# Kernel optimization log

Hardware: AMD Instinct MI355X
Metric: run time of the kernel (lower is better)

Reference implementation:

```python
import math
import jax, jax.numpy as jnp
from jax import lax
import numpy as np

SCORE_THR = 0.5
IOU_THR = 0.7
MIN_SIZE = 1.0
BBOX_CLIP = math.log(1000.0 / 16.0)

FEAT_SIZES = [100, 50, 25, 13, 7]
STRIDES = [8, 16, 32, 64, 128]
RATIOS = (0.5, 1.0, 2.0)
C = 256
A = 3
N = 2


def _make_priors(fs, stride):
    base = stride * 4.0
    ys, xs = np.meshgrid(np.arange(fs), np.arange(fs), indexing='ij')
    cx = (xs + 0.5) * stride
    cy = (ys + 0.5) * stride
    pri = []
    for r in RATIOS:
        w = base / np.sqrt(r)
        h = base * np.sqrt(r)
        pri.append(np.stack([cx - w / 2, cy - h / 2, cx + w / 2, cy + h / 2], axis=-1))
    pri = np.stack(pri, axis=2)  # (fs, fs, A, 4): H,W,A order matches permute/reshape
    return jnp.asarray(pri.reshape(-1, 4), dtype=jnp.float32)


def setup_inputs():
    key = jax.random.key(0)
    ks = jax.random.split(key, 8)
    inp = {}
    for i, fs in enumerate(FEAT_SIZES):
        inp[f'fmap{i}'] = jax.random.normal(jax.random.fold_in(ks[0], i), (N, C, fs, fs), dtype=jnp.float32)
        inp[f'priors{i}'] = _make_priors(fs, STRIDES[i])
    sc = 0.02
    inp['conv_w'] = jax.random.normal(ks[1], (C, C, 3, 3), jnp.float32) * sc
    inp['conv_b'] = jnp.zeros((C,), jnp.float32)
    inp['log_w'] = jax.random.normal(ks[2], (A, C, 1, 1), jnp.float32) * sc
    inp['log_b'] = jnp.zeros((A,), jnp.float32)
    inp['reg_w'] = jax.random.normal(ks[3], (A * 4, C, 1, 1), jnp.float32) * sc
    inp['reg_b'] = jnp.zeros((A * 4,), jnp.float32)
    inp['imsizes'] = jnp.full((N, 2), 800, dtype=jnp.int32)  # (h, w) per image
    inp['lvtop'] = 500
    inp['imtop'] = 100
    return inp


def _conv(x, w, b, pad):
    y = lax.conv_general_dilated(x, w, (1, 1), pad, dimension_numbers=('NCHW', 'OIHW', 'NCHW'))
    return y + b[None, :, None, None]


def _decode(reg, pri):
    pw = pri[..., 2] - pri[..., 0]
    ph = pri[..., 3] - pri[..., 1]
    pcx = pri[..., 0] + 0.5 * pw
    pcy = pri[..., 1] + 0.5 * ph
    dx, dy = reg[..., 0], reg[..., 1]
    dw = jnp.minimum(reg[..., 2], BBOX_CLIP)
    dh = jnp.minimum(reg[..., 3], BBOX_CLIP)
    cx = dx * pw + pcx
    cy = dy * ph + pcy
    w = jnp.exp(dw) * pw
    h = jnp.exp(dh) * ph
    return jnp.stack([cx - 0.5 * w, cy - 0.5 * h, cx + 0.5 * w, cy + 0.5 * h], axis=-1)


def _head(x, priors, conv_w, conv_b, log_w, log_b, reg_w, reg_b, lvtop):
    n = x.shape[0]
    h = jax.nn.relu(_conv(x, conv_w, conv_b, 'SAME'))
    reg = _conv(h, reg_w, reg_b, 'VALID').transpose(0, 2, 3, 1).reshape(n, -1, 4)
    log = _conv(h, log_w, log_b, 'VALID').transpose(0, 2, 3, 1).reshape(n, -1)
    k = min(lvtop, log.shape[1])
    vals, top = lax.top_k(log, k)                           # (n, k)
    reg = jnp.take_along_axis(reg, top[..., None], axis=1)  # (n, k, 4)
    pri = priors[top]                                       # (n, k, 4)
    return _decode(reg, pri), vals, k


def _box_iou(a, b):
    area_a = (a[:, 2] - a[:, 0]) * (a[:, 3] - a[:, 1])
    area_b = (b[:, 2] - b[:, 0]) * (b[:, 3] - b[:, 1])
    lt = jnp.maximum(a[:, None, :2], b[None, :, :2])
    rb = jnp.minimum(a[:, None, 2:], b[None, :, 2:])
    wh = jnp.clip(rb - lt, 0.0)
    inter = wh[..., 0] * wh[..., 1]
    return inter / (area_a[:, None] + area_b[None, :] - inter + 1e-9)


def _forward(fmaps, priors, conv_w, conv_b, log_w, log_b, reg_w, reg_b, imsizes, lvtop, imtop):
    tups = [_head(x, p, conv_w, conv_b, log_w, log_b, reg_w, reg_b, lvtop)
            for x, p in zip(fmaps, priors)]
    boxes = jnp.concatenate([t[0] for t in tups], axis=1)                 # (n, D, 4)
    obj = jax.nn.sigmoid(jnp.concatenate([t[1] for t in tups], axis=1))   # (n, D)
    lvlen = jnp.asarray([t[2] for t in tups])
    n, D = obj.shape
    boxes = boxes.reshape(-1, 4)
    obj = obj.reshape(-1)
    K = n * D
    imidx = jnp.arange(K) // D
    valid = obj >= SCORE_THR                                # score filter (masked, not nonzero)
    hw = imsizes[imidx].astype(jnp.float32)                 # (K, 2) = (h, w)
    x1 = jnp.clip(boxes[:, 0], 0.0, hw[:, 1])
    y1 = jnp.clip(boxes[:, 1], 0.0, hw[:, 0])
    x2 = jnp.clip(boxes[:, 2], 0.0, hw[:, 1])
    y2 = jnp.clip(boxes[:, 3], 0.0, hw[:, 0])
    boxes = jnp.stack([x1, y1, x2, y2], axis=-1)
    valid &= (x2 - x1 >= MIN_SIZE) & (y2 - y1 >= MIN_SIZE)  # remove_small
    lvidx = jnp.searchsorted(jnp.cumsum(lvlen), jnp.arange(K) % D, side='right')
    groups = imidx * 10 + lvidx
    scores = jnp.where(valid, obj, -jnp.inf)
    order = jnp.argsort(-scores)                            # global score order; groups gate suppression
    b, g, v, ii = boxes[order], groups[order], valid[order], imidx[order]
    iou = _box_iou(b, b)                                    # (K, K)
    ar = jnp.arange(K)
    def body(i, keep):
        sup = (iou[i] > IOU_THR) & (g == g[i]) & (ar > i)
        return jnp.where(keep[i], keep & ~sup, keep)
    keep = lax.fori_loop(0, K, body, v)                     # greedy batched NMS
    def select(i):
        m = keep & (ii == i)
        sel = jnp.argsort(~m)[:imtop]                       # stable: kept boxes in score order
        val = m[sel]
        bx = jnp.where(val[:, None], b[sel], 0.0)
        ix = jnp.where(val, i, -1)
        return bx, ix
    bx, ix = jax.vmap(select)(jnp.arange(n))
    return bx.reshape(n * imtop, 4), ix.reshape(n * imtop)


def reference(fmap0, fmap1, fmap2, fmap3, fmap4, priors0, priors1, priors2, priors3, priors4,
              conv_w, conv_b, log_w, log_b, reg_w, reg_b, imsizes, lvtop, imtop):
    return _forward([fmap0, fmap1, fmap2, fmap3, fmap4],
                    [priors0, priors1, priors2, priors3, priors4],
                    conv_w, conv_b, log_w, log_b, reg_w, reg_b, imsizes, lvtop, imtop)
```

## Files before the change

kernel.cpp:

```cpp
#include <hip/hip_runtime.h>
#include <math.h>


#define N_IMG 2
#define C_CH  256
#define D_PER 2147
#define K_TOT 4294
#define K_PAD 8192
#define CONV_BLOCKS 1912
#define CPX 239

__constant__ int c_Ml[5]     = {30000, 7500, 1875, 507, 147};
__constant__ int c_kl[5]     = {500, 500, 500, 500, 147};
__constant__ int c_lvoff[5]  = {0, 500, 1000, 1500, 2000};
__constant__ int c_logoff[5] = {0, 60000, 75000, 78750, 79764};
__constant__ int c_regoff[5] = {0, 240000, 300000, 315000, 319056};
__constant__ int c_fs[5]     = {100, 50, 25, 13, 7};
__constant__ int c_npt[5]    = {13, 7, 4, 2, 1};
__constant__ int c_E[5]      = {10000, 2500, 625, 169, 49};
__constant__ int c_cumbl[6]  = {0, 1352, 1744, 1872, 1904, 1912};
__constant__ int c_hcum[6]   = {0, 157, 197, 207, 210, 211};
__constant__ size_t c_hoff[5] = {0, 5120000, 6400000, 6720000, 6806528};

__global__ void transpose_w_kernel(const float* __restrict__ w,
                                   double* __restrict__ wT2) {
  int i = blockIdx.x * 256 + threadIdx.x;
  if (i >= 589824) return;
  int q = i % 2304;
  int slab = i / 2304;
  int cobi = slab >> 6, ch = slab & 63;
  int ci = q / 576;
  int rem = q % 576;
  int tap = rem / 64, co = rem & 63;
  wT2[i] =
      (double)w[(size_t)(cobi * 64 + co) * 2304 + (ch * 4 + ci) * 9 + tap];
}

template <typename T>
__global__ __launch_bounds__(256) void conv_fused_kernel(
    const float* __restrict__ x0, const float* __restrict__ x1,
    const float* __restrict__ x2, const float* __restrict__ x3,
    const float* __restrict__ x4, const double* __restrict__ wT2,
    const float* __restrict__ bias, T* __restrict__ h) {
  __shared__ double s_in[4 * 120];
  __shared__ double s_w[2304];
  int tid = threadIdx.x;
  int bid = (blockIdx.x & 7) * CPX + (blockIdx.x >> 3);
  int l = 0;
  while (bid >= c_cumbl[l + 1]) ++l;
  int r = bid - c_cumbl[l];
  int fs = c_fs[l], npt = c_npt[l];
  int tiles = npt * npt;
  int tile = r % tiles;
  int cn = r / tiles;
  int cobi = cn & 3, n = cn >> 2;
  int ptx = tile % npt, pty = tile / npt;
  int px0 = ptx * 8, py0 = pty * 8;
  int E = fs * fs;
  const float* xl;
  switch (l) {
    case 0: xl = x0; break;
    case 1: xl = x1; break;
    case 2: xl = x2; break;
    case 3: xl = x3; break;
    default: xl = x4; break;
  }
  const float* xn = xl + (size_t)n * C_CH * E;
  T* hl = h + c_hoff[l];

  int tpx = tid & 15, tco = tid >> 4;
  int prow = tpx >> 1, pcol0 = (tpx & 1) * 4;

  int in_dst[2], in_src[2];
#pragma unroll
  for (int it = 0; it < 2; ++it) {
    int idx = tid + it * 256;
    in_dst[it] = -1;
    in_src[it] = -1;
    if (idx < 400) {
      int ci = idx / 100, rr2 = idx % 100;
      int hy = rr2 / 10, hx = rr2 % 10;
      int gy = py0 - 1 + hy, gx = px0 - 1 + hx;
      in_dst[it] = ci * 120 + hy * 12 + hx;
      if (gy >= 0 && gy < fs && gx >= 0 && gx < fs)
        in_src[it] = ci * E + gy * fs + gx;
    }
  }

  double acc[4][4];
#pragma unroll
  for (int i = 0; i < 4; i++)
#pragma unroll
    for (int j = 0; j < 4; j++) acc[i][j] = 0.0;

  const double2* wsrc0 = (const double2*)(wT2 + (size_t)cobi * 64 * 2304);

  for (int ch = 0; ch < 64; ++ch) {
    const float* xc = xn + (size_t)ch * 4 * E;
#pragma unroll
    for (int it = 0; it < 2; ++it) {
      if (in_dst[it] >= 0) {
        float v = (in_src[it] >= 0) ? xc[in_src[it]] : 0.f;
        s_in[in_dst[it]] = (double)v;
      }
    }
    {
      const double2* src = wsrc0 + (size_t)ch * 1152;
      double2* dst = (double2*)s_w;
#pragma unroll
      for (int k = 0; k < 5; k++) {
        int idx = tid + k * 256;
        if (idx < 1152) dst[idx] = src[idx];
      }
    }
    __syncthreads();
#pragma unroll
    for (int ci = 0; ci < 4; ++ci) {
      const double* inp = &s_in[ci * 120];
      const double* wpb = &s_w[ci * 576];
#pragma unroll
      for (int ky = 0; ky < 3; ++ky) {
        const double* ip = inp + (prow + ky) * 12 + pcol0;
        double2 a0 = *(const double2*)ip;
        double2 a1 = *(const double2*)(ip + 2);
        double2 a2 = *(const double2*)(ip + 4);
        double d6[6];
        d6[0] = a0.x; d6[1] = a0.y; d6[2] = a1.x;
        d6[3] = a1.y; d6[4] = a2.x; d6[5] = a2.y;
#pragma unroll
        for (int kx = 0; kx < 3; ++kx) {
          const double* wp = wpb + (ky * 3 + kx) * 64 + tco * 4;
          double2 wA = *(const double2*)wp;
          double2 wB = *(const double2*)(wp + 2);
          double w0 = wA.x, w1 = wA.y, w2 = wB.x, w3 = wB.y;
#pragma unroll
          for (int pj = 0; pj < 4; pj++) {
            double iv = d6[pj + kx];
            acc[0][pj] = fma(w0, iv, acc[0][pj]);
            acc[1][pj] = fma(w1, iv, acc[1][pj]);
            acc[2][pj] = fma(w2, iv, acc[2][pj]);
            acc[3][pj] = fma(w3, iv, acc[3][pj]);
          }
        }
      }
    }
    __syncthreads();
  }

  int gy = py0 + prow;
  if (gy < fs) {
#pragma unroll
    for (int coi = 0; coi < 4; ++coi) {
      int co = cobi * 64 + tco * 4 + coi;
      double bb = (double)bias[co];
#pragma unroll
      for (int pj = 0; pj < 4; pj++) {
        int gx = px0 + pcol0 + pj;
        if (gx < fs) {
          double v = acc[coi][pj] + bb;
          hl[((size_t)n * C_CH + co) * E + gy * fs + gx] = (T)fmax(v, 0.0);
        }
      }
    }
  }
}

template <typename T>
__global__ __launch_bounds__(256) void heads_fused_kernel(
    const T* __restrict__ h, const float* __restrict__ logw,
    const float* __restrict__ logb, const float* __restrict__ regw,
    const float* __restrict__ regb, double* __restrict__ logits,
    double* __restrict__ regs) {
  __shared__ float s_wh[256][16];
  __shared__ double s_red[4][15][64];
  int tid = threadIdx.x;
  int n = blockIdx.y;
  int cidx = blockIdx.x;
  int l = 0;
  while (cidx >= c_hcum[l + 1]) ++l;
  int chunk = cidx - c_hcum[l];
  int E = c_E[l];
  int px0 = chunk * 64;
  const T* hl = h + c_hoff[l];
  double* logits_l = logits + c_logoff[l];
  double* regs_l = regs + c_regoff[l];

  for (int idx = tid; idx < 4096; idx += 256) {
    int c = idx >> 4, j = idx & 15;
    float v = 0.f;
    if (j < 3) v = logw[j * 256 + c];
    else if (j < 15) v = regw[(j - 3) * 256 + c];
    s_wh[c][j] = v;
  }
  __syncthreads();

  int p = tid & 63, c4 = tid >> 6;
  int pix = px0 + p;
  bool act = pix < E;
  double acc[15];
#pragma unroll
  for (int j = 0; j < 15; j++) acc[j] = 0.0;
  if (act) {
    const T* hp = hl + ((size_t)n * C_CH + c4 * 64) * E + pix;
    for (int cc = 0; cc < 64; ++cc) {
      double hv = (double)hp[(size_t)cc * E];
      const float* wr = &s_wh[c4 * 64 + cc][0];
#pragma unroll
      for (int j = 0; j < 15; j++)
        acc[j] = fma((double)wr[j], hv, acc[j]);
    }
  }
#pragma unroll
  for (int j = 0; j < 15; j++) s_red[c4][j][p] = acc[j];
  __syncthreads();
  if (act) {
    int M = E * 3;
    for (int j = c4; j < 15; j += 4) {
      double v = s_red[0][j][p] + s_red[1][j][p] + s_red[2][j][p] +
                 s_red[3][j][p];
      if (j < 3) {
        logits_l[(size_t)n * M + pix * 3 + j] = v + (double)logb[j];
      } else {
        int rj = j - 3, a = rj >> 2, coord = rj & 3;
        regs_l[((size_t)n * M + pix * 3 + a) * 4 + coord] =
            v + (double)regb[rj];
      }
    }
  }
}

__device__ __forceinline__ unsigned long long d2key(double v) {
  unsigned long long ub = (unsigned long long)__double_as_longlong(v);
  return (ub >> 63) ? ~ub : (ub | 0x8000000000000000ull);
}

#define TK_CH 30
__global__ __launch_bounds__(1024) void topk_kernel(
    const double* __restrict__ logits, int* __restrict__ cand_anchor) {
  int bid = blockIdx.x;
  int n = bid / 5, l = bid % 5;
  int M = c_Ml[l], k = c_kl[l];
  const double* lg = logits + c_logoff[l] + (size_t)n * M;
  int tid = threadIdx.x;
  __shared__ int histw[16][256];
  __shared__ int hist[256];
  __shared__ unsigned long long s_prefix;
  __shared__ int s_r;
  if (tid == 0) { s_prefix = 0ull; s_r = k; }

  int chunk = (M + 1023) >> 10;
  int i0 = tid * chunk, i1 = min(M, i0 + chunk);
  int cnt = i1 - i0;
  if (cnt < 0) cnt = 0;
  unsigned long long kv[TK_CH];
#pragma unroll
  for (int q = 0; q < TK_CH; q++)
    if (q < cnt) kv[q] = d2key(lg[i0 + q]);
  int wid = tid >> 6;
  __syncthreads();

  for (int pass = 0; pass < 8; ++pass) {
    int shift = 56 - pass * 8;
    for (int i = tid; i < 4096; i += 1024) ((int*)histw)[i] = 0;
    __syncthreads();
    unsigned long long pfx = s_prefix;
    int rr = s_r;
#pragma unroll
    for (int q = 0; q < TK_CH; q++) {
      if (q < cnt) {
        unsigned long long u = kv[q];
        if (pass == 0 || (u >> (shift + 8)) == pfx)
          atomicAdd(&histw[wid][(int)((u >> shift) & 255ull)], 1);
      }
    }
    __syncthreads();
    if (tid < 256) {
      int s = 0;
#pragma unroll
      for (int w = 0; w < 16; w++) s += histw[w][tid];
      hist[tid] = s;
    }
    __syncthreads();
    if (tid == 0) {
      int s = 0, beta = 0;
      for (int b = 255; b >= 0; --b) {
        if (s + hist[b] >= rr) { beta = b; break; }
        s += hist[b];
      }
      s_prefix = (pfx << 8) | (unsigned long long)beta;
      s_r = rr - s;
    }
    __syncthreads();
  }
  unsigned long long T = s_prefix;
  int need = s_r;
  int cgt = 0, ceq = 0;
#pragma unroll
  for (int q = 0; q < TK_CH; q++) {
    if (q < cnt) {
      cgt += (kv[q] > T);
      ceq += (kv[q] == T);
    }
  }
  __shared__ int sgt[1024], seq[1024];
  sgt[tid] = cgt;
  seq[tid] = ceq;
  __syncthreads();
  for (int o = 1; o < 1024; o <<= 1) {
    int a = (tid >= o) ? sgt[tid - o] : 0;
    int b2 = (tid >= o) ? seq[tid - o] : 0;
    __syncthreads();
    sgt[tid] += a;
    seq[tid] += b2;
    __syncthreads();
  }
  int gt_total = sgt[1023];
  int pg = sgt[tid] - cgt, pe = seq[tid] - ceq;
  int base = n * D_PER + c_lvoff[l];
#pragma unroll
  for (int q = 0; q < TK_CH; q++) {
    if (q < cnt) {
      unsigned long long u = kv[q];
      if (u > T) {
        cand_anchor[base + (pg++)] = i0 + q;
      } else if (u == T) {
        if (pe < need) cand_anchor[base + gt_total + pe] = i0 + q;
        pe++;
      }
    }
  }
}

__global__ __launch_bounds__(256) void decode_kernel(
    const int* __restrict__ cand_anchor, const double* __restrict__ logits,
    const double* __restrict__ regs, const float* __restrict__ p0,
    const float* __restrict__ p1, const float* __restrict__ p2,
    const float* __restrict__ p3, const float* __restrict__ p4,
    const int* __restrict__ imsizes, double* __restrict__ cand_score,
    double* __restrict__ cand_box, int* __restrict__ cand_group,
    int* __restrict__ cand_valid) {
  int s = blockIdx.x * 256 + threadIdx.x;
  if (s >= K_TOT) return;
  int n = s / D_PER;
  int rr = s % D_PER;
  int l = (rr < 2000) ? (rr / 500) : 4;
  int aidx = cand_anchor[s];
  int M = c_Ml[l];
  const float* pp;
  switch (l) {
    case 0: pp = p0; break;
    case 1: pp = p1; break;
    case 2: pp = p2; break;
    case 3: pp = p3; break;
    default: pp = p4; break;
  }
  double lv = logits[c_logoff[l] + (size_t)n * M + aidx];
  double obj = 1.0 / (1.0 + exp(-lv));
  const double* rp = regs + c_regoff[l] + ((size_t)n * M + aidx) * 4;
  const float* pr = pp + (size_t)aidx * 4;
  double px1 = pr[0], py1 = pr[1], px2 = pr[2], py2 = pr[3];
  double pw = px2 - px1, ph = py2 - py1;
  double pcx = px1 + 0.5 * pw, pcy = py1 + 0.5 * ph;
  const double BCLIP = 4.1351665567423560;
  double dx = rp[0], dy = rp[1];
  double dw = fmin(rp[2], BCLIP), dh = fmin(rp[3], BCLIP);
  double cx = dx * pw + pcx, cy = dy * ph + pcy;
  double w = exp(dw) * pw, hh = exp(dh) * ph;
  double x1 = cx - 0.5 * w, y1 = cy - 0.5 * hh;
  double x2 = cx + 0.5 * w, y2 = cy + 0.5 * hh;
  double imh = (double)imsizes[n * 2 + 0], imw = (double)imsizes[n * 2 + 1];
  x1 = fmin(fmax(x1, 0.0), imw);
  x2 = fmin(fmax(x2, 0.0), imw);
  y1 = fmin(fmax(y1, 0.0), imh);
  y2 = fmin(fmax(y2, 0.0), imh);
  bool valid = (obj >= 0.5) && ((x2 - x1) >= 1.0) && ((y2 - y1) >= 1.0);
  cand_box[(size_t)s * 4 + 0] = x1;
  cand_box[(size_t)s * 4 + 1] = y1;
  cand_box[(size_t)s * 4 + 2] = x2;
  cand_box[(size_t)s * 4 + 3] = y2;
  cand_score[s] = valid ? obj : -(double)INFINITY;
  cand_group[s] = n * 5 + l;
  cand_valid[s] = valid ? 1 : 0;
}

__global__ __launch_bounds__(1024) void sort_kernel(
    const double* __restrict__ cand_score, int* __restrict__ order) {
  __shared__ unsigned long long key[K_PAD];
  int tid = threadIdx.x;
  for (int i = tid; i < K_PAD; i += 1024) {
    unsigned long long kk = 0ull;
    if (i < K_TOT) {
      unsigned long long u = d2key(cand_score[i]);
      kk = (u & ~0x1FFFull) | (unsigned long long)i;
    }
    key[i] = kk;
  }
  __syncthreads();
  for (int k = 2; k <= K_PAD; k <<= 1) {
    for (int j = k >> 1; j > 0; j >>= 1) {
      for (int i = tid; i < K_PAD; i += 1024) {
        int ixj = i ^ j;
        if (ixj > i) {
          unsigned long long a = key[i], b = key[ixj];
          bool sw = ((i & k) == 0) ? (a < b) : (a > b);
          if (sw) { key[i] = b; key[ixj] = a; }
        }
      }
      __syncthreads();
    }
  }
  for (int i = tid; i < K_TOT; i += 1024)
    order[i] = (int)(key[i] & 0x1FFFull);
}

__global__ __launch_bounds__(256) void gather_kernel(
    const int* __restrict__ order, const double* __restrict__ cand_box,
    const int* __restrict__ cand_group, const int* __restrict__ cand_valid,
    double* __restrict__ box_s, int* __restrict__ grp_s,
    int* __restrict__ img_s, int* __restrict__ valid_s,
    int* __restrict__ keep_s) {
  int i = blockIdx.x * 256 + threadIdx.x;
  if (i >= K_TOT) return;
  int s = order[i];
#pragma unroll
  for (int q = 0; q < 4; q++)
    box_s[(size_t)i * 4 + q] = cand_box[(size_t)s * 4 + q];
  int g = cand_group[s];
  grp_s[i] = g;
  img_s[i] = g / 5;
  valid_s[i] = cand_valid[s];
  keep_s[i] = 0;
}

#define MAXM 512
__global__ __launch_bounds__(256) void nms_kernel(
    const double* __restrict__ box_s, const int* __restrict__ grp_s,
    const int* __restrict__ valid_s, int* __restrict__ keep_s) {
  int g = blockIdx.x;
  int tid = threadIdx.x;
  __shared__ int cnt[256];
  __shared__ int mem[MAXM];
  __shared__ double bx[MAXM][4];
  __shared__ unsigned long long mask[MAXM][8];
  const int chunk = (K_TOT + 255) / 256;
  int i0 = tid * chunk, i1 = min(K_TOT, i0 + chunk);
  int c = 0;
  for (int i = i0; i < i1; ++i) c += (grp_s[i] == g && valid_s[i]);
  cnt[tid] = c;
  __syncthreads();
  for (int o = 1; o < 256; o <<= 1) {
    int v = (tid >= o) ? cnt[tid - o] : 0;
    __syncthreads();
    cnt[tid] += v;
    __syncthreads();
  }
  int off = cnt[tid] - c;
  int m = cnt[255];
  for (int i = i0; i < i1; ++i)
    if (grp_s[i] == g && valid_s[i]) mem[off++] = i;
  __syncthreads();
  for (int t = tid; t < m; t += 256) {
    int i = mem[t];
#pragma unroll
    for (int q = 0; q < 4; q++) bx[t][q] = box_s[(size_t)i * 4 + q];
  }
  __syncthreads();
  for (int i = tid; i < m; i += 256) {
    unsigned long long row[8] = {0, 0, 0, 0, 0, 0, 0, 0};
    double ax1 = bx[i][0], ay1 = bx[i][1], ax2 = bx[i][2], ay2 = bx[i][3];
    double areaA = (ax2 - ax1) * (ay2 - ay1);
    for (int j = i + 1; j < m; ++j) {
      double bx1 = bx[j][0], by1 = bx[j][1], bx2 = bx[j][2], by2 = bx[j][3];
      double areaB = (bx2 - bx1) * (by2 - by1);
      double lx = fmax(ax1, bx1), ly = fmax(ay1, by1);
      double rx = fmin(ax2, bx2), ry = fmin(ay2, by2);
      double iw = fmax(rx - lx, 0.0), ih = fmax(ry - ly, 0.0);
      double inter = iw * ih;
      double iou = inter / (areaA + areaB - inter + 1e-9);
      if (iou > 0.7) row[j >> 6] |= (1ull << (j & 63));
    }
#pragma unroll
    for (int w2 = 0; w2 < 8; ++w2) mask[i][w2] = row[w2];
  }
  __syncthreads();
  if (tid == 0) {
    unsigned long long remv[8] = {0, 0, 0, 0, 0, 0, 0, 0};
    for (int i = 0; i < m; ++i) {
      if (!((remv[i >> 6] >> (i & 63)) & 1ull)) {
        keep_s[mem[i]] = 1;
#pragma unroll
        for (int w2 = 0; w2 < 8; ++w2) remv[w2] |= mask[i][w2];
      }
    }
  }
}

__global__ __launch_bounds__(256) void select_kernel(
    const double* __restrict__ box_s, const int* __restrict__ img_s,
    const int* __restrict__ keep_s, float* __restrict__ out) {
  int n = blockIdx.x;
  int tid = threadIdx.x;
  __shared__ int cnt[256];
  const int chunk = (K_TOT + 255) / 256;
  int i0 = tid * chunk, i1 = min(K_TOT, i0 + chunk);
  int c = 0;
  for (int i = i0; i < i1; ++i) c += (keep_s[i] && img_s[i] == n);
  cnt[tid] = c;
  __syncthreads();
  for (int o = 1; o < 256; o <<= 1) {
    int v = (tid >= o) ? cnt[tid - o] : 0;
    __syncthreads();
    cnt[tid] += v;
    __syncthreads();
  }
  int pos = cnt[tid] - c;
  int total = cnt[255];
  for (int i = i0; i < i1; ++i) {
    if (keep_s[i] && img_s[i] == n) {
      if (pos < 100) {
#pragma unroll
        for (int q = 0; q < 4; q++)
          out[(n * 100 + pos) * 4 + q] = (float)box_s[(size_t)i * 4 + q];
        out[800 + n * 100 + pos] = (float)n;
      }
      pos++;
    }
  }
  for (int p = total + tid; p < 100; p += 256) {
#pragma unroll
    for (int q = 0; q < 4; q++) out[(n * 100 + p) * 4 + q] = 0.0f;
    out[800 + n * 100 + p] = -1.0f;
  }
}

extern "C" void kernel_launch(void* const* d_in, const int* in_sizes, int n_in,
                              void* d_out, int out_size, void* d_ws,
                              size_t ws_size, hipStream_t stream) {
  (void)in_sizes; (void)n_in; (void)out_size;
  const float* fmap[5];
  const float* priors[5];
  for (int l = 0; l < 5; l++) {
    fmap[l] = (const float*)d_in[2 * l];
    priors[l] = (const float*)d_in[2 * l + 1];
  }
  const float* conv_w = (const float*)d_in[10];
  const float* conv_b = (const float*)d_in[11];
  const float* log_w = (const float*)d_in[12];
  const float* log_b = (const float*)d_in[13];
  const float* reg_w = (const float*)d_in[14];
  const float* reg_b = (const float*)d_in[15];
  const int* imsizes = (const int*)d_in[16];
  float* out = (float*)d_out;

  bool f64h = ws_size >= (size_t)66000000;

  char* base = (char*)d_ws;
  size_t off = 0;
  auto alloc = [&](size_t bytes) -> void* {
    off = (off + 255) & ~(size_t)255;
    void* p = base + off;
    off += bytes;
    return p;
  };
  double* wT2 = (double*)alloc(589824ull * 8);
  void* hraw = alloc(6831616ull * (f64h ? 8 : 4));
  double* logits = (double*)alloc(80058ull * 8);
  double* regs = (double*)alloc(320232ull * 8);
  int* cand_anchor = (int*)alloc(K_TOT * 4);
  double* cand_score = (double*)alloc(K_TOT * 8);
  double* cand_box = (double*)alloc((size_t)K_TOT * 4 * 8);
  int* cand_group = (int*)alloc(K_TOT * 4);
  int* cand_valid = (int*)alloc(K_TOT * 4);
  int* order = (int*)alloc(K_TOT * 4);
  double* box_s = (double*)alloc((size_t)K_TOT * 4 * 8);
  int* grp_s = (int*)alloc(K_TOT * 4);
  int* img_s = (int*)alloc(K_TOT * 4);
  int* valid_s = (int*)alloc(K_TOT * 4);
  int* keep_s = (int*)alloc(K_TOT * 4);

  transpose_w_kernel<<<2304, 256, 0, stream>>>(conv_w, wT2);

  if (f64h) {
    conv_fused_kernel<double><<<CONV_BLOCKS, 256, 0, stream>>>(
        fmap[0], fmap[1], fmap[2], fmap[3], fmap[4], wT2, conv_b,
        (double*)hraw);
    heads_fused_kernel<double><<<dim3(211, 2), 256, 0, stream>>>(
        (double*)hraw, log_w, log_b, reg_w, reg_b, logits, regs);
  } else {
    conv_fused_kernel<float><<<CONV_BLOCKS, 256, 0, stream>>>(
        fmap[0], fmap[1], fmap[2], fmap[3], fmap[4], wT2, conv_b,
        (float*)hraw);
    heads_fused_kernel<float><<<dim3(211, 2), 256, 0, stream>>>(
        (float*)hraw, log_w, log_b, reg_w, reg_b, logits, regs);
  }
  topk_kernel<<<10, 1024, 0, stream>>>(logits, cand_anchor);
  decode_kernel<<<(K_TOT + 255) / 256, 256, 0, stream>>>(
      cand_anchor, logits, regs, priors[0], priors[1], priors[2], priors[3],
      priors[4], imsizes, cand_score, cand_box, cand_group, cand_valid);
  sort_kernel<<<1, 1024, 0, stream>>>(cand_score, order);
  gather_kernel<<<(K_TOT + 255) / 256, 256, 0, stream>>>(
      order, cand_box, cand_group, cand_valid, box_s, grp_s, img_s, valid_s,
      keep_s);
  nms_kernel<<<10, 256, 0, stream>>>(box_s, grp_s, valid_s, keep_s);
  select_kernel<<<2, 256, 0, stream>>>(box_s, img_s, keep_s, out);
}
```

Measured before the change: 1.199 ms.

## Fuse topk, decode, per-group sort and NMS into one kernel; merge-select per image

Replaces the topk, decode, global 8192-wide bitonic sort, gather and NMS kernels with one kernel per (image, level) group. Each block does its own top-k, decodes boxes into shared memory, sorts 512 keys locally and runs NMS, then writes the kept boxes in order. A 5-way merge in select_kernel then builds the per-image top 100. The conv input tile stride also changes from 12 to 13 doubles, presumably to cut LDS bank conflicts, which gives up the aligned double2 loads. The intent is to cut launch count, global round-trips and the large single-block sort in the post-processing tail.

```diff
diff --git a/kernel.cpp b/kernel.cpp
--- a/kernel.cpp
+++ b/kernel.cpp
@@ -6,13 +6,11 @@
 #define C_CH  256
 #define D_PER 2147
 #define K_TOT 4294
-#define K_PAD 8192
 #define CONV_BLOCKS 1912
 #define CPX 239
 
 __constant__ int c_Ml[5]     = {30000, 7500, 1875, 507, 147};
 __constant__ int c_kl[5]     = {500, 500, 500, 500, 147};
-__constant__ int c_lvoff[5]  = {0, 500, 1000, 1500, 2000};
 __constant__ int c_logoff[5] = {0, 60000, 75000, 78750, 79764};
 __constant__ int c_regoff[5] = {0, 240000, 300000, 315000, 319056};
 __constant__ int c_fs[5]     = {100, 50, 25, 13, 7};
@@ -42,7 +40,7 @@
     const float* __restrict__ x2, const float* __restrict__ x3,
     const float* __restrict__ x4, const double* __restrict__ wT2,
     const float* __restrict__ bias, T* __restrict__ h) {
-  __shared__ double s_in[4 * 120];
+  __shared__ double s_in[4 * 130];
   __shared__ double s_w[2304];
   int tid = threadIdx.x;
   int bid = (blockIdx.x & 7) * CPX + (blockIdx.x >> 3);
@@ -81,7 +79,7 @@
       int ci = idx / 100, rr2 = idx % 100;
       int hy = rr2 / 10, hx = rr2 % 10;
       int gy = py0 - 1 + hy, gx = px0 - 1 + hx;
-      in_dst[it] = ci * 120 + hy * 12 + hx;
+      in_dst[it] = ci * 130 + hy * 13 + hx;
       if (gy >= 0 && gy < fs && gx >= 0 && gx < fs)
         in_src[it] = ci * E + gy * fs + gx;
     }
@@ -99,10 +97,8 @@
     const float* xc = xn + (size_t)ch * 4 * E;
 #pragma unroll
     for (int it = 0; it < 2; ++it) {
-      if (in_dst[it] >= 0) {
-        float v = (in_src[it] >= 0) ? xc[in_src[it]] : 0.f;
-        s_in[in_dst[it]] = (double)v;
-      }
+      if (in_dst[it] >= 0)
+        s_in[in_dst[it]] = (in_src[it] >= 0) ? (double)xc[in_src[it]] : 0.0;
     }
     {
       const double2* src = wsrc0 + (size_t)ch * 1152;
@@ -116,17 +112,14 @@
     __syncthreads();
 #pragma unroll
     for (int ci = 0; ci < 4; ++ci) {
-      const double* inp = &s_in[ci * 120];
+      const double* inp = &s_in[ci * 130];
       const double* wpb = &s_w[ci * 576];
 #pragma unroll
       for (int ky = 0; ky < 3; ++ky) {
-        const double* ip = inp + (prow + ky) * 12 + pcol0;
-        double2 a0 = *(const double2*)ip;
-        double2 a1 = *(const double2*)(ip + 2);
-        double2 a2 = *(const double2*)(ip + 4);
+        const double* ip = inp + (prow + ky) * 13 + pcol0;
         double d6[6];
-        d6[0] = a0.x; d6[1] = a0.y; d6[2] = a1.x;
-        d6[3] = a1.y; d6[4] = a2.x; d6[5] = a2.y;
+#pragma unroll
+        for (int j = 0; j < 6; j++) d6[j] = ip[j];
 #pragma unroll
         for (int kx = 0; kx < 3; ++kx) {
           const double* wp = wpb + (ky * 3 + kx) * 64 + tco * 4;
@@ -235,17 +228,40 @@
 }
 
 #define TK_CH 30
-__global__ __launch_bounds__(1024) void topk_kernel(
-    const double* __restrict__ logits, int* __restrict__ cand_anchor) {
+union TkShared {
+  struct {
+    int histw[16][256];
+    int hist[256];
+    int sgt[1024];
+    int seq[1024];
+  } a;
+  struct {
+    unsigned long long u[512];
+    int idx[512];
+    int keep[512];
+    int ps[512];
+    int m;
+    double bx[512][4];
+    unsigned long long mask[512][8];
+  } b;
+};
+
+__global__ __launch_bounds__(1024) void topk_nms_kernel(
+    const double* __restrict__ logits, const double* __restrict__ regs,
+    const float* __restrict__ p0, const float* __restrict__ p1,
+    const float* __restrict__ p2, const float* __restrict__ p3,
+    const float* __restrict__ p4, const int* __restrict__ imsizes,
+    double* __restrict__ g_box, unsigned long long* __restrict__ g_u,
+    int* __restrict__ g_cnt) {
+  __shared__ TkShared sh;
+  __shared__ int s_sel[512];
+  __shared__ unsigned long long s_prefix;
+  __shared__ int s_r;
   int bid = blockIdx.x;
   int n = bid / 5, l = bid % 5;
   int M = c_Ml[l], k = c_kl[l];
   const double* lg = logits + c_logoff[l] + (size_t)n * M;
   int tid = threadIdx.x;
-  __shared__ int histw[16][256];
-  __shared__ int hist[256];
-  __shared__ unsigned long long s_prefix;
-  __shared__ int s_r;
   if (tid == 0) { s_prefix = 0ull; s_r = k; }
 
   int chunk = (M + 1023) >> 10;
@@ -261,7 +277,7 @@
 
   for (int pass = 0; pass < 8; ++pass) {
     int shift = 56 - pass * 8;
-    for (int i = tid; i < 4096; i += 1024) ((int*)histw)[i] = 0;
+    for (int i = tid; i < 4096; i += 1024) ((int*)sh.a.histw)[i] = 0;
     __syncthreads();
     unsigned long long pfx = s_prefix;
     int rr = s_r;
@@ -270,22 +286,22 @@
       if (q < cnt) {
         unsigned long long u = kv[q];
         if (pass == 0 || (u >> (shift + 8)) == pfx)
-          atomicAdd(&histw[wid][(int)((u >> shift) & 255ull)], 1);
+          atomicAdd(&sh.a.histw[wid][(int)((u >> shift) & 255ull)], 1);
       }
     }
     __syncthreads();
     if (tid < 256) {
       int s = 0;
 #pragma unroll
-      for (int w = 0; w < 16; w++) s += histw[w][tid];
-      hist[tid] = s;
+      for (int w = 0; w < 16; w++) s += sh.a.histw[w][tid];
+      sh.a.hist[tid] = s;
     }
     __syncthreads();
     if (tid == 0) {
       int s = 0, beta = 0;
       for (int b = 255; b >= 0; --b) {
-        if (s + hist[b] >= rr) { beta = b; break; }
-        s += hist[b];
+        if (s + sh.a.hist[b] >= rr) { beta = b; break; }
+        s += sh.a.hist[b];
       }
       s_prefix = (pfx << 8) | (unsigned long long)beta;
       s_r = rr - s;
@@ -302,50 +318,33 @@
       ceq += (kv[q] == T);
     }
   }
-  __shared__ int sgt[1024], seq[1024];
-  sgt[tid] = cgt;
-  seq[tid] = ceq;
+  sh.a.sgt[tid] = cgt;
+  sh.a.seq[tid] = ceq;
   __syncthreads();
   for (int o = 1; o < 1024; o <<= 1) {
-    int a = (tid >= o) ? sgt[tid - o] : 0;
-    int b2 = (tid >= o) ? seq[tid - o] : 0;
-    __syncthreads();
-    sgt[tid] += a;
-    seq[tid] += b2;
-    __syncthreads();
-  }
-  int gt_total = sgt[1023];
-  int pg = sgt[tid] - cgt, pe = seq[tid] - ceq;
-  int base = n * D_PER + c_lvoff[l];
+    int a = (tid >= o) ? sh.a.sgt[tid - o] : 0;
+    int b2 = (tid >= o) ? sh.a.seq[tid - o] : 0;
+    __syncthreads();
+    sh.a.sgt[tid] += a;
+    sh.a.seq[tid] += b2;
+    __syncthreads();
+  }
+  int gt_total = sh.a.sgt[1023];
+  int pg = sh.a.sgt[tid] - cgt, pe = sh.a.seq[tid] - ceq;
 #pragma unroll
   for (int q = 0; q < TK_CH; q++) {
     if (q < cnt) {
       unsigned long long u = kv[q];
       if (u > T) {
-        cand_anchor[base + (pg++)] = i0 + q;
+        s_sel[pg++] = i0 + q;
       } else if (u == T) {
-        if (pe < need) cand_anchor[base + gt_total + pe] = i0 + q;
+        if (pe < need) s_sel[gt_total + pe] = i0 + q;
         pe++;
       }
     }
   }
-}
-
-__global__ __launch_bounds__(256) void decode_kernel(
-    const int* __restrict__ cand_anchor, const double* __restrict__ logits,
-    const double* __restrict__ regs, const float* __restrict__ p0,
-    const float* __restrict__ p1, const float* __restrict__ p2,
-    const float* __restrict__ p3, const float* __restrict__ p4,
-    const int* __restrict__ imsizes, double* __restrict__ cand_score,
-    double* __restrict__ cand_box, int* __restrict__ cand_group,
-    int* __restrict__ cand_valid) {
-  int s = blockIdx.x * 256 + threadIdx.x;
-  if (s >= K_TOT) return;
-  int n = s / D_PER;
-  int rr = s % D_PER;
-  int l = (rr < 2000) ? (rr / 500) : 4;
-  int aidx = cand_anchor[s];
-  int M = c_Ml[l];
+  __syncthreads();
+
   const float* pp;
   switch (l) {
     case 0: pp = p0; break;
@@ -354,123 +353,79 @@
     case 3: pp = p3; break;
     default: pp = p4; break;
   }
-  double lv = logits[c_logoff[l] + (size_t)n * M + aidx];
-  double obj = 1.0 / (1.0 + exp(-lv));
-  const double* rp = regs + c_regoff[l] + ((size_t)n * M + aidx) * 4;
-  const float* pr = pp + (size_t)aidx * 4;
-  double px1 = pr[0], py1 = pr[1], px2 = pr[2], py2 = pr[3];
-  double pw = px2 - px1, ph = py2 - py1;
-  double pcx = px1 + 0.5 * pw, pcy = py1 + 0.5 * ph;
+  const double* regs_l = regs + c_regoff[l];
+  double imh = (double)imsizes[n * 2 + 0], imw = (double)imsizes[n * 2 + 1];
   const double BCLIP = 4.1351665567423560;
-  double dx = rp[0], dy = rp[1];
-  double dw = fmin(rp[2], BCLIP), dh = fmin(rp[3], BCLIP);
-  double cx = dx * pw + pcx, cy = dy * ph + pcy;
-  double w = exp(dw) * pw, hh = exp(dh) * ph;
-  double x1 = cx - 0.5 * w, y1 = cy - 0.5 * hh;
-  double x2 = cx + 0.5 * w, y2 = cy + 0.5 * hh;
-  double imh = (double)imsizes[n * 2 + 0], imw = (double)imsizes[n * 2 + 1];
-  x1 = fmin(fmax(x1, 0.0), imw);
-  x2 = fmin(fmax(x2, 0.0), imw);
-  y1 = fmin(fmax(y1, 0.0), imh);
-  y2 = fmin(fmax(y2, 0.0), imh);
-  bool valid = (obj >= 0.5) && ((x2 - x1) >= 1.0) && ((y2 - y1) >= 1.0);
-  cand_box[(size_t)s * 4 + 0] = x1;
-  cand_box[(size_t)s * 4 + 1] = y1;
-  cand_box[(size_t)s * 4 + 2] = x2;
-  cand_box[(size_t)s * 4 + 3] = y2;
-  cand_score[s] = valid ? obj : -(double)INFINITY;
-  cand_group[s] = n * 5 + l;
-  cand_valid[s] = valid ? 1 : 0;
-}
-
-__global__ __launch_bounds__(1024) void sort_kernel(
-    const double* __restrict__ cand_score, int* __restrict__ order) {
-  __shared__ unsigned long long key[K_PAD];
-  int tid = threadIdx.x;
-  for (int i = tid; i < K_PAD; i += 1024) {
-    unsigned long long kk = 0ull;
-    if (i < K_TOT) {
-      unsigned long long u = d2key(cand_score[i]);
-      kk = (u & ~0x1FFFull) | (unsigned long long)i;
-    }
-    key[i] = kk;
-  }
-  __syncthreads();
-  for (int k = 2; k <= K_PAD; k <<= 1) {
-    for (int j = k >> 1; j > 0; j >>= 1) {
-      for (int i = tid; i < K_PAD; i += 1024) {
-        int ixj = i ^ j;
+  if (tid < 512) {
+    unsigned long long key = 0ull;
+    sh.b.idx[tid] = tid;
+    sh.b.keep[tid] = 0;
+    if (tid < k) {
+      int aidx = s_sel[tid];
+      double lv = lg[aidx];
+      double obj = 1.0 / (1.0 + exp(-lv));
+      const double* rp = regs_l + ((size_t)n * M + aidx) * 4;
+      const float* pr = pp + (size_t)aidx * 4;
+      double px1 = pr[0], py1 = pr[1], px2 = pr[2], py2 = pr[3];
+      double pw = px2 - px1, ph = py2 - py1;
+      double pcx = px1 + 0.5 * pw, pcy = py1 + 0.5 * ph;
+      double dx = rp[0], dy = rp[1];
+      double dw = fmin(rp[2], BCLIP), dh = fmin(rp[3], BCLIP);
+      double cx = dx * pw + pcx, cy = dy * ph + pcy;
+      double w = exp(dw) * pw, hh = exp(dh) * ph;
+      double x1 = cx - 0.5 * w, y1 = cy - 0.5 * hh;
+      double x2 = cx + 0.5 * w, y2 = cy + 0.5 * hh;
+      x1 = fmin(fmax(x1, 0.0), imw);
+      x2 = fmin(fmax(x2, 0.0), imw);
+      y1 = fmin(fmax(y1, 0.0), imh);
+      y2 = fmin(fmax(y2, 0.0), imh);
+      bool valid = (obj >= 0.5) && ((x2 - x1) >= 1.0) && ((y2 - y1) >= 1.0);
+      sh.b.bx[tid][0] = x1;
+      sh.b.bx[tid][1] = y1;
+      sh.b.bx[tid][2] = x2;
+      sh.b.bx[tid][3] = y2;
+      if (valid) key = d2key(obj);
+    }
+    sh.b.u[tid] = key;
+  }
+  if (tid == 0) sh.b.m = 0;
+  __syncthreads();
+
+  for (int kk = 2; kk <= 512; kk <<= 1) {
+    for (int j = kk >> 1; j > 0; j >>= 1) {
+      if (tid < 512) {
+        int i = tid, ixj = i ^ j;
         if (ixj > i) {
-          unsigned long long a = key[i], b = key[ixj];
-          bool sw = ((i & k) == 0) ? (a < b) : (a > b);
-          if (sw) { key[i] = b; key[ixj] = a; }
+          unsigned long long ua = sh.b.u[i], ub = sh.b.u[ixj];
+          int ia = sh.b.idx[i], ib = sh.b.idx[ixj];
+          bool up = ((i & kk) == 0);
+          bool aAfterB = (ua < ub) || (ua == ub && ia > ib);
+          bool sw = up ? aAfterB : !aAfterB && (ua != ub || ia != ib);
+          if (sw) {
+            sh.b.u[i] = ub; sh.b.u[ixj] = ua;
+            sh.b.idx[i] = ib; sh.b.idx[ixj] = ia;
+          }
         }
       }
       __syncthreads();
     }
   }
-  for (int i = tid; i < K_TOT; i += 1024)
-    order[i] = (int)(key[i] & 0x1FFFull);
-}
-
-__global__ __launch_bounds__(256) void gather_kernel(
-    const int* __restrict__ order, const double* __restrict__ cand_box,
-    const int* __restrict__ cand_group, const int* __restrict__ cand_valid,
-    double* __restrict__ box_s, int* __restrict__ grp_s,
-    int* __restrict__ img_s, int* __restrict__ valid_s,
-    int* __restrict__ keep_s) {
-  int i = blockIdx.x * 256 + threadIdx.x;
-  if (i >= K_TOT) return;
-  int s = order[i];
-#pragma unroll
-  for (int q = 0; q < 4; q++)
-    box_s[(size_t)i * 4 + q] = cand_box[(size_t)s * 4 + q];
-  int g = cand_group[s];
-  grp_s[i] = g;
-  img_s[i] = g / 5;
-  valid_s[i] = cand_valid[s];
-  keep_s[i] = 0;
-}
-
-#define MAXM 512
-__global__ __launch_bounds__(256) void nms_kernel(
-    const double* __restrict__ box_s, const int* __restrict__ grp_s,
-    const int* __restrict__ valid_s, int* __restrict__ keep_s) {
-  int g = blockIdx.x;
-  int tid = threadIdx.x;
-  __shared__ int cnt[256];
-  __shared__ int mem[MAXM];
-  __shared__ double bx[MAXM][4];
-  __shared__ unsigned long long mask[MAXM][8];
-  const int chunk = (K_TOT + 255) / 256;
-  int i0 = tid * chunk, i1 = min(K_TOT, i0 + chunk);
-  int c = 0;
-  for (int i = i0; i < i1; ++i) c += (grp_s[i] == g && valid_s[i]);
-  cnt[tid] = c;
-  __syncthreads();
-  for (int o = 1; o < 256; o <<= 1) {
-    int v = (tid >= o) ? cnt[tid - o] : 0;
-    __syncthreads();
-    cnt[tid] += v;
-    __syncthreads();
-  }
-  int off = cnt[tid] - c;
-  int m = cnt[255];
-  for (int i = i0; i < i1; ++i)
-    if (grp_s[i] == g && valid_s[i]) mem[off++] = i;
-  __syncthreads();
-  for (int t = tid; t < m; t += 256) {
-    int i = mem[t];
-#pragma unroll
-    for (int q = 0; q < 4; q++) bx[t][q] = box_s[(size_t)i * 4 + q];
-  }
-  __syncthreads();
-  for (int i = tid; i < m; i += 256) {
+  if (tid < 512) {
+    if (sh.b.u[tid] != 0ull && (tid == 511 || sh.b.u[tid + 1] == 0ull))
+      sh.b.m = tid + 1;
+  }
+  __syncthreads();
+  int m = sh.b.m;
+
+  if (tid < 512 && tid < m) {
+    int i = tid;
+    const double* A = sh.b.bx[sh.b.idx[i]];
+    double ax1 = A[0], ay1 = A[1], ax2 = A[2], ay2 = A[3];
+    double areaA = (ax2 - ax1) * (ay2 - ay1);
     unsigned long long row[8] = {0, 0, 0, 0, 0, 0, 0, 0};
-    double ax1 = bx[i][0], ay1 = bx[i][1], ax2 = bx[i][2], ay2 = bx[i][3];
-    double areaA = (ax2 - ax1) * (ay2 - ay1);
     for (int j = i + 1; j < m; ++j) {
-      double bx1 = bx[j][0], by1 = bx[j][1], bx2 = bx[j][2], by2 = bx[j][3];
+      const double* B = sh.b.bx[sh.b.idx[j]];
+      double bx1 = B[0], by1 = B[1], bx2 = B[2], by2 = B[3];
       double areaB = (bx2 - bx1) * (by2 - by1);
       double lx = fmax(ax1, bx1), ly = fmax(ay1, by1);
       double rx = fmin(ax2, bx2), ry = fmin(ay2, by2);
@@ -480,56 +435,92 @@
       if (iou > 0.7) row[j >> 6] |= (1ull << (j & 63));
     }
 #pragma unroll
-    for (int w2 = 0; w2 < 8; ++w2) mask[i][w2] = row[w2];
-  }
-  __syncthreads();
+    for (int w2 = 0; w2 < 8; ++w2) sh.b.mask[i][w2] = row[w2];
+  }
+  __syncthreads();
+
   if (tid == 0) {
     unsigned long long remv[8] = {0, 0, 0, 0, 0, 0, 0, 0};
     for (int i = 0; i < m; ++i) {
       if (!((remv[i >> 6] >> (i & 63)) & 1ull)) {
-        keep_s[mem[i]] = 1;
-#pragma unroll
-        for (int w2 = 0; w2 < 8; ++w2) remv[w2] |= mask[i][w2];
-      }
-    }
-  }
+        sh.b.keep[i] = 1;
+#pragma unroll
+        for (int w2 = 0; w2 < 8; ++w2) remv[w2] |= sh.b.mask[i][w2];
+      }
+    }
+  }
+  __syncthreads();
+
+  if (tid < 512) sh.b.ps[tid] = sh.b.keep[tid];
+  __syncthreads();
+  for (int o = 1; o < 512; o <<= 1) {
+    int v = 0;
+    if (tid < 512 && tid >= o) v = sh.b.ps[tid - o];
+    __syncthreads();
+    if (tid < 512) sh.b.ps[tid] += v;
+    __syncthreads();
+  }
+  if (tid < 512 && sh.b.keep[tid]) {
+    int pos = sh.b.ps[tid] - 1;
+    const double* B = sh.b.bx[sh.b.idx[tid]];
+    size_t gbase = (size_t)bid * 512 + pos;
+#pragma unroll
+    for (int q = 0; q < 4; q++) g_box[gbase * 4 + q] = B[q];
+    g_u[gbase] = sh.b.u[tid];
+  }
+  if (tid == 0) g_cnt[bid] = (m > 0) ? sh.b.ps[511] : 0;
 }
 
 __global__ __launch_bounds__(256) void select_kernel(
-    const double* __restrict__ box_s, const int* __restrict__ img_s,
-    const int* __restrict__ keep_s, float* __restrict__ out) {
+    const double* __restrict__ g_box, const unsigned long long* __restrict__ g_u,
+    const int* __restrict__ g_cnt, float* __restrict__ out) {
+  __shared__ unsigned long long s_u[5][512];
+  __shared__ int s_pick[100];
+  __shared__ int s_total;
   int n = blockIdx.x;
   int tid = threadIdx.x;
-  __shared__ int cnt[256];
-  const int chunk = (K_TOT + 255) / 256;
-  int i0 = tid * chunk, i1 = min(K_TOT, i0 + chunk);
-  int c = 0;
-  for (int i = i0; i < i1; ++i) c += (keep_s[i] && img_s[i] == n);
-  cnt[tid] = c;
-  __syncthreads();
-  for (int o = 1; o < 256; o <<= 1) {
-    int v = (tid >= o) ? cnt[tid - o] : 0;
-    __syncthreads();
-    cnt[tid] += v;
-    __syncthreads();
-  }
-  int pos = cnt[tid] - c;
-  int total = cnt[255];
-  for (int i = i0; i < i1; ++i) {
-    if (keep_s[i] && img_s[i] == n) {
-      if (pos < 100) {
-#pragma unroll
-        for (int q = 0; q < 4; q++)
-          out[(n * 100 + pos) * 4 + q] = (float)box_s[(size_t)i * 4 + q];
-        out[800 + n * 100 + pos] = (float)n;
-      }
-      pos++;
-    }
-  }
-  for (int p = total + tid; p < 100; p += 256) {
-#pragma unroll
-    for (int q = 0; q < 4; q++) out[(n * 100 + p) * 4 + q] = 0.0f;
-    out[800 + n * 100 + p] = -1.0f;
+  int cnts[5];
+#pragma unroll
+  for (int l = 0; l < 5; l++) cnts[l] = g_cnt[n * 5 + l];
+  for (int idx = tid; idx < 5 * 512; idx += 256) {
+    int l = idx >> 9, r = idx & 511;
+    s_u[l][r] = (r < cnts[l]) ? g_u[(size_t)(n * 5 + l) * 512 + r] : 0ull;
+  }
+  __syncthreads();
+  if (tid == 0) {
+    int hd[5] = {0, 0, 0, 0, 0};
+    int t = 0;
+    while (t < 100) {
+      int bl = -1;
+      unsigned long long bu = 0ull;
+      for (int l = 0; l < 5; l++) {
+        if (hd[l] < cnts[l] && s_u[l][hd[l]] > bu) {
+          bu = s_u[l][hd[l]];
+          bl = l;
+        }
+      }
+      if (bl < 0) break;
+      s_pick[t++] = bl * 512 + hd[bl];
+      hd[bl]++;
+    }
+    s_total = t;
+  }
+  __syncthreads();
+  int total = s_total;
+  for (int t = tid; t < 100; t += 256) {
+    if (t < total) {
+      int pk = s_pick[t];
+      int l = pk >> 9, r = pk & 511;
+      size_t gbase = (size_t)(n * 5 + l) * 512 + r;
+#pragma unroll
+      for (int q = 0; q < 4; q++)
+        out[(n * 100 + t) * 4 + q] = (float)g_box[gbase * 4 + q];
+      out[800 + n * 100 + t] = (float)n;
+    } else {
+#pragma unroll
+      for (int q = 0; q < 4; q++) out[(n * 100 + t) * 4 + q] = 0.0f;
+      out[800 + n * 100 + t] = -1.0f;
+    }
   }
 }
 
@@ -566,17 +557,9 @@
   void* hraw = alloc(6831616ull * (f64h ? 8 : 4));
   double* logits = (double*)alloc(80058ull * 8);
   double* regs = (double*)alloc(320232ull * 8);
-  int* cand_anchor = (int*)alloc(K_TOT * 4);
-  double* cand_score = (double*)alloc(K_TOT * 8);
-  double* cand_box = (double*)alloc((size_t)K_TOT * 4 * 8);
-  int* cand_group = (int*)alloc(K_TOT * 4);
-  int* cand_valid = (int*)alloc(K_TOT * 4);
-  int* order = (int*)alloc(K_TOT * 4);
-  double* box_s = (double*)alloc((size_t)K_TOT * 4 * 8);
-  int* grp_s = (int*)alloc(K_TOT * 4);
-  int* img_s = (int*)alloc(K_TOT * 4);
-  int* valid_s = (int*)alloc(K_TOT * 4);
-  int* keep_s = (int*)alloc(K_TOT * 4);
+  double* g_box = (double*)alloc(10ull * 512 * 4 * 8);
+  unsigned long long* g_u = (unsigned long long*)alloc(10ull * 512 * 8);
+  int* g_cnt = (int*)alloc(10 * 4);
 
   transpose_w_kernel<<<2304, 256, 0, stream>>>(conv_w, wT2);
 
@@ -593,14 +576,8 @@
     heads_fused_kernel<float><<<dim3(211, 2), 256, 0, stream>>>(
         (float*)hraw, log_w, log_b, reg_w, reg_b, logits, regs);
   }
-  topk_kernel<<<10, 1024, 0, stream>>>(logits, cand_anchor);
-  decode_kernel<<<(K_TOT + 255) / 256, 256, 0, stream>>>(
-      cand_anchor, logits, regs, priors[0], priors[1], priors[2], priors[3],
-      priors[4], imsizes, cand_score, cand_box, cand_group, cand_valid);
-  sort_kernel<<<1, 1024, 0, stream>>>(cand_score, order);
-  gather_kernel<<<(K_TOT + 255) / 256, 256, 0, stream>>>(
-      order, cand_box, cand_group, cand_valid, box_s, grp_s, img_s, valid_s,
-      keep_s);
-  nms_kernel<<<10, 256, 0, stream>>>(box_s, grp_s, valid_s, keep_s);
-  select_kernel<<<2, 256, 0, stream>>>(box_s, img_s, keep_s, out);
-}
+  topk_nms_kernel<<<10, 1024, 0, stream>>>(
+      logits, regs, priors[0], priors[1], priors[2], priors[3], priors[4],
+      imsizes, g_box, g_u, g_cnt);
+  select_kernel<<<2, 256, 0, stream>>>(g_box, g_u, g_cnt, out);
+}
```

Measured after the change: 1.262 ms. 5.2% more time.
